# Kernel tuning notes

Measured on AMD Instinct MI355X. Metric: run time of the kernel, lower is better.

## Reference

```python
import jax, jax.numpy as jnp
import numpy as np

N_NODES = 100000
N_EDGES = 3200000
NEG_SLOPE = 0.01  # torch F.leaky_relu default


def _spmm(edge_src, edge_dst, edge_vals, x):
    # out[i] = sum_{e: dst[e]==i} vals[e] * x[src[e]]  ==  A @ x for COO A
    msgs = edge_vals[:, None] * x[edge_src]  # [E, D]
    return jax.ops.segment_sum(msgs, edge_dst, num_segments=N_NODES)


def _gcn_layer(x, edge_src, edge_dst, edge_vals, W, b):
    h = x @ W                      # dense GEMM [N, out]
    h = _spmm(edge_src, edge_dst, edge_vals, h)  # sparse aggregation
    h = h + b
    return jax.nn.leaky_relu(h, NEG_SLOPE)  # dropout=0 -> no-op


def setup_inputs() -> dict:
    key = jax.random.key(0)
    ks = jax.random.split(key, 10)
    nfeat, hid, ncls = 512, 256, 40
    features = jax.random.normal(ks[0], (N_NODES, nfeat), dtype=jnp.float32)
    edge_src = jax.random.randint(ks[1], (N_EDGES,), 0, N_NODES, dtype=jnp.int32)
    edge_dst = jax.random.randint(ks[2], (N_EDGES,), 0, N_NODES, dtype=jnp.int32)
    edge_vals = jax.random.uniform(ks[3], (N_EDGES,), dtype=jnp.float32)
    # init like torch: uniform(-stdv, stdv), stdv = 1/sqrt(out_features)
    def uinit(k, shape, out):
        s = 1.0 / np.sqrt(out)
        return jax.random.uniform(k, shape, minval=-s, maxval=s, dtype=jnp.float32)
    return {
        "features": features,
        "edge_src": edge_src,
        "edge_dst": edge_dst,
        "edge_vals": edge_vals,
        "W1": uinit(ks[4], (nfeat, hid), hid),
        "b1": uinit(ks[5], (hid,), hid),
        "Wh": uinit(ks[6], (hid, hid), hid),
        "bh": uinit(ks[7], (hid,), hid),
        "W2": uinit(ks[8], (hid, ncls), ncls),
        "b2": uinit(ks[9], (ncls,), ncls),
    }


def reference(features, edge_src, edge_dst, edge_vals, W1, b1, Wh, bh, W2, b2):
    x = _gcn_layer(features, edge_src, edge_dst, edge_vals, W1, b1)
    x = _gcn_layer(x, edge_src, edge_dst, edge_vals, Wh, bh)
    # output layer also uses default use_activation=True in the source
    x = _gcn_layer(x, edge_src, edge_dst, edge_vals, W2, b2)
    return x  # [N_NODES, nclasses]
```

## Files before the change

### kernel.cpp

```cpp
#include <hip/hip_runtime.h>

#define NEG_SLOPE 0.01f

typedef __attribute__((ext_vector_type(8))) short bf16x8;
typedef __attribute__((ext_vector_type(4))) float f32x4;

static __device__ __forceinline__ unsigned short f2bf(float f) {
  unsigned int u = __float_as_uint(f);
  return (unsigned short)((u + 0x7fffu + ((u >> 16) & 1u)) >> 16);
}
static __device__ __forceinline__ float bf2f(unsigned short s) {
  return __uint_as_float(((unsigned int)s) << 16);
}
static __device__ __forceinline__ float leaky(float r) { return r > 0.f ? r : r * NEG_SLOPE; }


__global__ __launch_bounds__(256) void zero_int_kernel(int* __restrict__ p, int n) {
  int i = blockIdx.x * 256 + threadIdx.x;
  if (i < n) p[i] = 0;
}

__global__ __launch_bounds__(256) void hist_kernel(const int* __restrict__ dst, int* __restrict__ cnt, int E) {
  int i = blockIdx.x * 256 + threadIdx.x;
  if (i < E) atomicAdd(&cnt[dst[i]], 1);
}

__global__ __launch_bounds__(256) void scan1_kernel(const int* __restrict__ cnt, int* __restrict__ rp,
                                                    int* __restrict__ bsum, int n) {
  __shared__ int sh[256];
  int t = threadIdx.x;
  int base = blockIdx.x * 2048 + t * 8;
  int v[8];
  int tot = 0;
#pragma unroll
  for (int j = 0; j < 8; ++j) {
    int i = base + j;
    int c = (i < n) ? cnt[i] : 0;
    v[j] = tot;
    tot += c;
  }
  sh[t] = tot;
  __syncthreads();
  for (int off = 1; off < 256; off <<= 1) {
    int x = sh[t];
    int y = (t >= off) ? sh[t - off] : 0;
    __syncthreads();
    sh[t] = x + y;
    __syncthreads();
  }
  int pre = sh[t] - tot;
#pragma unroll
  for (int j = 0; j < 8; ++j) {
    int i = base + j;
    if (i < n) rp[i] = pre + v[j];
  }
  if (t == 255) bsum[blockIdx.x] = sh[255];
}

__global__ void scan2_kernel(int* __restrict__ bsum, int nb, int* __restrict__ rp, int n) {
  if (threadIdx.x == 0 && blockIdx.x == 0) {
    int run = 0;
    for (int i = 0; i < nb; ++i) {
      int t = bsum[i];
      bsum[i] = run;
      run += t;
    }
    rp[n] = run;
  }
}

__global__ __launch_bounds__(256) void scan3_kernel(int* __restrict__ rp, const int* __restrict__ bsum,
                                                    int* __restrict__ cursor, int n) {
  int i = blockIdx.x * 256 + threadIdx.x;
  if (i < n) {
    int v = rp[i] + bsum[i >> 11];
    rp[i] = v;
    cursor[i] = v;
  }
}

__global__ __launch_bounds__(256) void scatter_kernel(const int* __restrict__ src, const int* __restrict__ dst,
                                                      const float* __restrict__ vals, int* __restrict__ cursor,
                                                      int* __restrict__ csrc, float* __restrict__ cval, int E) {
  int i = blockIdx.x * 256 + threadIdx.x;
  if (i < E) {
    int d = dst[i];
    int pos = atomicAdd(&cursor[d], 1);
    csrc[pos] = src[i];
    cval[pos] = vals[i];
  }
}


__global__ __launch_bounds__(256) void cvt_w_kernel(const float* __restrict__ W, unsigned short* __restrict__ Wt,
                                                    int K, int Nreal, int Npad) {
  int i = blockIdx.x * 256 + threadIdx.x;
  if (i >= Npad * K) return;
  int n = i / K, k = i - n * K;
  float v = (n < Nreal) ? W[(size_t)k * Nreal + n] : 0.f;
  Wt[i] = f2bf(v);
}


__global__ __launch_bounds__(256) void gemm_mfma_kernel(const float* __restrict__ A, const unsigned short* __restrict__ Wt,
                                                        unsigned short* __restrict__ C, int M, int N, int K) {
  __shared__ __align__(16) short As[128 * 72];
  __shared__ __align__(16) short Bs[64 * 72];
  const int t = threadIdx.x;
  const int lane = t & 63;
  const int w = t >> 6;
  const int wr = w >> 1;
  const int wc = w & 1;
  const int row0 = blockIdx.x * 128;
  const int col0 = blockIdx.y * 64;
  const int l15 = lane & 15;
  const int l16 = lane >> 4;

  f32x4 acc[4][2];
#pragma unroll
  for (int m = 0; m < 4; ++m)
#pragma unroll
    for (int n = 0; n < 2; ++n) acc[m][n] = (f32x4){0.f, 0.f, 0.f, 0.f};

  for (int k0 = 0; k0 < K; k0 += 64) {
    __syncthreads();
#pragma unroll
    for (int it = 0; it < 8; ++it) {
      int idx = it * 256 + t;
      int row = idx >> 4;
      int c4 = idx & 15;
      int grow = row0 + row;
      float4 v = make_float4(0.f, 0.f, 0.f, 0.f);
      if (grow < M) v = *(const float4*)&A[(size_t)grow * K + k0 + c4 * 4];
      unsigned int lo = (unsigned int)f2bf(v.x) | ((unsigned int)f2bf(v.y) << 16);
      unsigned int hi = (unsigned int)f2bf(v.z) | ((unsigned int)f2bf(v.w) << 16);
      *(uint2*)&As[row * 72 + c4 * 4] = make_uint2(lo, hi);
    }
#pragma unroll
    for (int it = 0; it < 2; ++it) {
      int idx = it * 256 + t;
      int n = idx >> 3;
      int c8 = idx & 7;
      uint4 v = *(const uint4*)&Wt[(size_t)(col0 + n) * K + k0 + c8 * 8];
      *(uint4*)&Bs[n * 72 + c8 * 8] = v;
    }
    __syncthreads();
#pragma unroll
    for (int kk = 0; kk < 64; kk += 32) {
      bf16x8 a[4], b[2];
#pragma unroll
      for (int m = 0; m < 4; ++m)
        a[m] = *(const bf16x8*)&As[(wr * 64 + m * 16 + l15) * 72 + kk + l16 * 8];
#pragma unroll
      for (int n = 0; n < 2; ++n)
        b[n] = *(const bf16x8*)&Bs[(wc * 32 + n * 16 + l15) * 72 + kk + l16 * 8];
#pragma unroll
      for (int m = 0; m < 4; ++m)
#pragma unroll
        for (int n = 0; n < 2; ++n)
          acc[m][n] = __builtin_amdgcn_mfma_f32_16x16x32_bf16(a[m], b[n], acc[m][n], 0, 0, 0);
    }
  }
#pragma unroll
  for (int m = 0; m < 4; ++m) {
#pragma unroll
    for (int j = 0; j < 4; ++j) {
      int grow = row0 + wr * 64 + m * 16 + l16 * 4 + j;
      if (grow < M) {
#pragma unroll
        for (int n = 0; n < 2; ++n) {
          int gcol = col0 + wc * 32 + n * 16 + l15;
          C[(size_t)grow * N + gcol] = f2bf(acc[m][n][j]);
        }
      }
    }
  }
}


__global__ __launch_bounds__(256) void spmm_d256_kernel(const unsigned short* __restrict__ x, const int* __restrict__ rp,
                                                        const int* __restrict__ csrc, const float* __restrict__ cval,
                                                        const float* __restrict__ bias, float* __restrict__ out, int n) {
  int node = blockIdx.x * 4 + (threadIdx.x >> 6);
  int lane = threadIdx.x & 63;
  if (node >= n) return;
  int s = rp[node], e = rp[node + 1];
  float a0 = 0.f, a1 = 0.f, a2 = 0.f, a3 = 0.f;
  int p = s;
  for (; p + 8 <= e; p += 8) {
    int srcs[8];
    float vals[8];
    uint2 rv[8];
#pragma unroll
    for (int q = 0; q < 8; ++q) {
      srcs[q] = csrc[p + q];
      vals[q] = cval[p + q];
    }
#pragma unroll
    for (int q = 0; q < 8; ++q)
      rv[q] = *(const uint2*)((const char*)x + (size_t)srcs[q] * 512 + lane * 8);
#pragma unroll
    for (int q = 0; q < 8; ++q) {
      a0 = fmaf(vals[q], __uint_as_float(rv[q].x << 16), a0);
      a1 = fmaf(vals[q], __uint_as_float(rv[q].x & 0xffff0000u), a1);
      a2 = fmaf(vals[q], __uint_as_float(rv[q].y << 16), a2);
      a3 = fmaf(vals[q], __uint_as_float(rv[q].y & 0xffff0000u), a3);
    }
  }
  for (; p < e; ++p) {
    int s0 = csrc[p];
    float v0 = cval[p];
    uint2 r = *(const uint2*)((const char*)x + (size_t)s0 * 512 + lane * 8);
    a0 = fmaf(v0, __uint_as_float(r.x << 16), a0);
    a1 = fmaf(v0, __uint_as_float(r.x & 0xffff0000u), a1);
    a2 = fmaf(v0, __uint_as_float(r.y << 16), a2);
    a3 = fmaf(v0, __uint_as_float(r.y & 0xffff0000u), a3);
  }
  float4 b = *(const float4*)&bias[lane * 4];
  float4 o;
  o.x = leaky(a0 + b.x);
  o.y = leaky(a1 + b.y);
  o.z = leaky(a2 + b.z);
  o.w = leaky(a3 + b.w);
  *(float4*)&out[(size_t)node * 256 + lane * 4] = o;
}


__global__ __launch_bounds__(256) void spmm_small_kernel(const unsigned short* __restrict__ x, const int* __restrict__ rp,
                                                         const int* __restrict__ csrc, const float* __restrict__ cval,
                                                         const float* __restrict__ bias, float* __restrict__ out,
                                                         int n, int D, int ldx) {
  int node = blockIdx.x * 4 + (threadIdx.x >> 6);
  int lane = threadIdx.x & 63;
  if (node >= n) return;
  int l = lane < D ? lane : 0;
  int s = rp[node], e = rp[node + 1];
  float acc = 0.f;
  int p = s;
  for (; p + 4 <= e; p += 4) {
    int s0 = csrc[p], s1 = csrc[p + 1], s2 = csrc[p + 2], s3 = csrc[p + 3];
    float v0 = cval[p], v1 = cval[p + 1], v2 = cval[p + 2], v3 = cval[p + 3];
    acc = fmaf(v0, bf2f(x[(size_t)s0 * ldx + l]), acc);
    acc = fmaf(v1, bf2f(x[(size_t)s1 * ldx + l]), acc);
    acc = fmaf(v2, bf2f(x[(size_t)s2 * ldx + l]), acc);
    acc = fmaf(v3, bf2f(x[(size_t)s3 * ldx + l]), acc);
  }
  for (; p < e; ++p) acc = fmaf(cval[p], bf2f(x[(size_t)csrc[p] * ldx + l]), acc);
  if (lane < D) {
    out[(size_t)node * D + lane] = leaky(acc + bias[lane]);
  }
}


extern "C" void kernel_launch(void* const* d_in, const int* in_sizes, int n_in,
                              void* d_out, int out_size, void* d_ws, size_t ws_size,
                              hipStream_t stream) {
  const float* features = (const float*)d_in[0];
  const int* esrc = (const int*)d_in[1];
  const int* edst = (const int*)d_in[2];
  const float* evals = (const float*)d_in[3];
  const float* W1 = (const float*)d_in[4];
  const float* b1 = (const float*)d_in[5];
  const float* Wh = (const float*)d_in[6];
  const float* bh = (const float*)d_in[7];
  const float* W2 = (const float*)d_in[8];
  const float* b2 = (const float*)d_in[9];

  const int E = in_sizes[1];
  const int hid = in_sizes[5];
  const int ncls = in_sizes[9];
  const int nfeat = in_sizes[4] / hid;
  const int Nn = in_sizes[0] / nfeat;
  const int nclsPad = 64;

  char* ws = (char*)d_ws;
  size_t off = 0;
  auto alloc = [&](size_t bytes) {
    char* p = ws + off;
    off += (bytes + 255) & ~(size_t)255;
    return p;
  };
  unsigned short* hA = (unsigned short*)alloc((size_t)Nn * hid * 2);
  float* hB = (float*)alloc((size_t)Nn * hid * 4);
  unsigned short* g3 = (unsigned short*)alloc((size_t)Nn * nclsPad * 2);
  unsigned short* Wt1 = (unsigned short*)alloc((size_t)hid * nfeat * 2);
  unsigned short* Wt2 = (unsigned short*)alloc((size_t)hid * hid * 2);
  unsigned short* Wt3 = (unsigned short*)alloc((size_t)nclsPad * hid * 2);
  int* rp = (int*)alloc((size_t)(Nn + 1) * 4);
  int* cursor = (int*)alloc((size_t)Nn * 4);
  int nb = (Nn + 2047) / 2048;
  int* bsum = (int*)alloc((size_t)nb * 4);
  int* csrc = (int*)alloc((size_t)E * 4);
  float* cval = (float*)alloc((size_t)E * 4);
  (void)ws_size;

  dim3 blk(256);

  zero_int_kernel<<<(Nn + 255) / 256, blk, 0, stream>>>(cursor, Nn);
  hist_kernel<<<(E + 255) / 256, blk, 0, stream>>>(edst, cursor, E);
  scan1_kernel<<<nb, blk, 0, stream>>>(cursor, rp, bsum, Nn);
  scan2_kernel<<<1, 64, 0, stream>>>(bsum, nb, rp, Nn);
  scan3_kernel<<<(Nn + 255) / 256, blk, 0, stream>>>(rp, bsum, cursor, Nn);
  scatter_kernel<<<(E + 255) / 256, blk, 0, stream>>>(esrc, edst, evals, cursor, csrc, cval, E);

  cvt_w_kernel<<<(hid * nfeat + 255) / 256, blk, 0, stream>>>(W1, Wt1, nfeat, hid, hid);
  cvt_w_kernel<<<(hid * hid + 255) / 256, blk, 0, stream>>>(Wh, Wt2, hid, hid, hid);
  cvt_w_kernel<<<(nclsPad * hid + 255) / 256, blk, 0, stream>>>(W2, Wt3, hid, ncls, nclsPad);

  int gm = (Nn + 127) / 128;

  gemm_mfma_kernel<<<dim3(gm, hid / 64), blk, 0, stream>>>(features, Wt1, hA, Nn, hid, nfeat);
  spmm_d256_kernel<<<(Nn + 3) / 4, blk, 0, stream>>>(hA, rp, csrc, cval, b1, hB, Nn);

  gemm_mfma_kernel<<<dim3(gm, hid / 64), blk, 0, stream>>>(hB, Wt2, hA, Nn, hid, hid);
  spmm_d256_kernel<<<(Nn + 3) / 4, blk, 0, stream>>>(hA, rp, csrc, cval, bh, hB, Nn);

  gemm_mfma_kernel<<<dim3(gm, nclsPad / 64), blk, 0, stream>>>(hB, Wt3, g3, Nn, nclsPad, hid);
  spmm_small_kernel<<<(Nn + 3) / 4, blk, 0, stream>>>(g3, rp, csrc, cval, b2, (float*)d_out, Nn, ncls, nclsPad);
}
```

Measured before the change: 1.378 ms.

## Store hidden activations as bf16 and widen GEMM tile to full output width

The SpMM kernels now write their hidden-layer outputs as bf16 instead of fp32, so the next GEMM reads half the bytes and loads them into shared memory without conversion. The GEMM is templated so one block covers all output columns (256 wide with 8 waves, or 64 wide with 2 waves). Each A row tile is then read from global memory once rather than once per column block. This cuts the redundant re-reads of features and hidden activations, at the cost of more accumulator registers per wave, fewer blocks, and an extra bf16 rounding of intermediate activations.

```diff
diff --git a/kernel.cpp b/kernel.cpp
--- a/kernel.cpp
+++ b/kernel.cpp
@@ -102,62 +102,76 @@
 }
 
 
-__global__ __launch_bounds__(256) void gemm_mfma_kernel(const float* __restrict__ A, const unsigned short* __restrict__ Wt,
-                                                        unsigned short* __restrict__ C, int M, int N, int K) {
+template <int BN, int WN, bool A_F32>
+__global__ __launch_bounds__(128 * WN) void gemm_bf16_kernel(const void* __restrict__ Ap,
+                                                             const unsigned short* __restrict__ Wt,
+                                                             unsigned short* __restrict__ C, int M, int K) {
+  constexpr int THREADS = 128 * WN;
   __shared__ __align__(16) short As[128 * 72];
-  __shared__ __align__(16) short Bs[64 * 72];
+  __shared__ __align__(16) short Bs[BN * 72];
   const int t = threadIdx.x;
   const int lane = t & 63;
   const int w = t >> 6;
-  const int wr = w >> 1;
-  const int wc = w & 1;
+  const int wr = w / WN;
+  const int wc = w % WN;
   const int row0 = blockIdx.x * 128;
-  const int col0 = blockIdx.y * 64;
   const int l15 = lane & 15;
   const int l16 = lane >> 4;
 
-  f32x4 acc[4][2];
+  f32x4 acc[4][4];
 #pragma unroll
   for (int m = 0; m < 4; ++m)
 #pragma unroll
-    for (int n = 0; n < 2; ++n) acc[m][n] = (f32x4){0.f, 0.f, 0.f, 0.f};
+    for (int n = 0; n < 4; ++n) acc[m][n] = (f32x4){0.f, 0.f, 0.f, 0.f};
 
   for (int k0 = 0; k0 < K; k0 += 64) {
     __syncthreads();
-#pragma unroll
-    for (int it = 0; it < 8; ++it) {
-      int idx = it * 256 + t;
-      int row = idx >> 4;
-      int c4 = idx & 15;
-      int grow = row0 + row;
-      float4 v = make_float4(0.f, 0.f, 0.f, 0.f);
-      if (grow < M) v = *(const float4*)&A[(size_t)grow * K + k0 + c4 * 4];
-      unsigned int lo = (unsigned int)f2bf(v.x) | ((unsigned int)f2bf(v.y) << 16);
-      unsigned int hi = (unsigned int)f2bf(v.z) | ((unsigned int)f2bf(v.w) << 16);
-      *(uint2*)&As[row * 72 + c4 * 4] = make_uint2(lo, hi);
-    }
-#pragma unroll
-    for (int it = 0; it < 2; ++it) {
-      int idx = it * 256 + t;
-      int n = idx >> 3;
-      int c8 = idx & 7;
-      uint4 v = *(const uint4*)&Wt[(size_t)(col0 + n) * K + k0 + c8 * 8];
+    if constexpr (A_F32) {
+      const float* A = (const float*)Ap;
+#pragma unroll
+      for (int it = 0; it < 2048 / THREADS; ++it) {
+        int idx = it * THREADS + t;
+        int row = idx >> 4, c4 = idx & 15;
+        int grow = row0 + row;
+        float4 v = make_float4(0.f, 0.f, 0.f, 0.f);
+        if (grow < M) v = *(const float4*)&A[(size_t)grow * K + k0 + c4 * 4];
+        unsigned int lo = (unsigned int)f2bf(v.x) | ((unsigned int)f2bf(v.y) << 16);
+        unsigned int hi = (unsigned int)f2bf(v.z) | ((unsigned int)f2bf(v.w) << 16);
+        *(uint2*)&As[row * 72 + c4 * 4] = make_uint2(lo, hi);
+      }
+    } else {
+      const unsigned short* A = (const unsigned short*)Ap;
+#pragma unroll
+      for (int it = 0; it < 1024 / THREADS; ++it) {
+        int idx = it * THREADS + t;
+        int row = idx >> 3, c8 = idx & 7;
+        int grow = row0 + row;
+        uint4 v = make_uint4(0u, 0u, 0u, 0u);
+        if (grow < M) v = *(const uint4*)&A[(size_t)grow * K + c8 * 8 + k0];
+        *(uint4*)&As[row * 72 + c8 * 8] = v;
+      }
+    }
+#pragma unroll
+    for (int it = 0; it < BN * 8 / THREADS; ++it) {
+      int idx = it * THREADS + t;
+      int n = idx >> 3, c8 = idx & 7;
+      uint4 v = *(const uint4*)&Wt[(size_t)n * K + k0 + c8 * 8];
       *(uint4*)&Bs[n * 72 + c8 * 8] = v;
     }
     __syncthreads();
 #pragma unroll
     for (int kk = 0; kk < 64; kk += 32) {
-      bf16x8 a[4], b[2];
+      bf16x8 a[4], b[4];
 #pragma unroll
       for (int m = 0; m < 4; ++m)
         a[m] = *(const bf16x8*)&As[(wr * 64 + m * 16 + l15) * 72 + kk + l16 * 8];
 #pragma unroll
-      for (int n = 0; n < 2; ++n)
-        b[n] = *(const bf16x8*)&Bs[(wc * 32 + n * 16 + l15) * 72 + kk + l16 * 8];
+      for (int n = 0; n < 4; ++n)
+        b[n] = *(const bf16x8*)&Bs[(wc * 64 + n * 16 + l15) * 72 + kk + l16 * 8];
 #pragma unroll
       for (int m = 0; m < 4; ++m)
 #pragma unroll
-        for (int n = 0; n < 2; ++n)
+        for (int n = 0; n < 4; ++n)
           acc[m][n] = __builtin_amdgcn_mfma_f32_16x16x32_bf16(a[m], b[n], acc[m][n], 0, 0, 0);
     }
   }
@@ -168,9 +182,9 @@
       int grow = row0 + wr * 64 + m * 16 + l16 * 4 + j;
       if (grow < M) {
 #pragma unroll
-        for (int n = 0; n < 2; ++n) {
-          int gcol = col0 + wc * 32 + n * 16 + l15;
-          C[(size_t)grow * N + gcol] = f2bf(acc[m][n][j]);
+        for (int n = 0; n < 4; ++n) {
+          int gcol = wc * 64 + n * 16 + l15;
+          C[(size_t)grow * BN + gcol] = f2bf(acc[m][n][j]);
         }
       }
     }
@@ -180,7 +194,8 @@
 
 __global__ __launch_bounds__(256) void spmm_d256_kernel(const unsigned short* __restrict__ x, const int* __restrict__ rp,
                                                         const int* __restrict__ csrc, const float* __restrict__ cval,
-                                                        const float* __restrict__ bias, float* __restrict__ out, int n) {
+                                                        const float* __restrict__ bias, unsigned short* __restrict__ out,
+                                                        int n) {
   int node = blockIdx.x * 4 + (threadIdx.x >> 6);
   int lane = threadIdx.x & 63;
   if (node >= n) return;
@@ -217,12 +232,9 @@
     a3 = fmaf(v0, __uint_as_float(r.y & 0xffff0000u), a3);
   }
   float4 b = *(const float4*)&bias[lane * 4];
-  float4 o;
-  o.x = leaky(a0 + b.x);
-  o.y = leaky(a1 + b.y);
-  o.z = leaky(a2 + b.z);
-  o.w = leaky(a3 + b.w);
-  *(float4*)&out[(size_t)node * 256 + lane * 4] = o;
+  unsigned int o01 = (unsigned int)f2bf(leaky(a0 + b.x)) | ((unsigned int)f2bf(leaky(a1 + b.y)) << 16);
+  unsigned int o23 = (unsigned int)f2bf(leaky(a2 + b.z)) | ((unsigned int)f2bf(leaky(a3 + b.w)) << 16);
+  *(uint2*)&out[(size_t)node * 256 + lane * 4] = make_uint2(o01, o23);
 }
 
 
@@ -281,7 +293,7 @@
     return p;
   };
   unsigned short* hA = (unsigned short*)alloc((size_t)Nn * hid * 2);
-  float* hB = (float*)alloc((size_t)Nn * hid * 4);
+  unsigned short* hB = (unsigned short*)alloc((size_t)Nn * hid * 2);
   unsigned short* g3 = (unsigned short*)alloc((size_t)Nn * nclsPad * 2);
   unsigned short* Wt1 = (unsigned short*)alloc((size_t)hid * nfeat * 2);
   unsigned short* Wt2 = (unsigned short*)alloc((size_t)hid * hid * 2);
@@ -309,12 +321,12 @@
 
   int gm = (Nn + 127) / 128;
 
-  gemm_mfma_kernel<<<dim3(gm, hid / 64), blk, 0, stream>>>(features, Wt1, hA, Nn, hid, nfeat);
+  gemm_bf16_kernel<256, 4, true><<<dim3(gm, 1), dim3(512), 0, stream>>>(features, Wt1, hA, Nn, nfeat);
   spmm_d256_kernel<<<(Nn + 3) / 4, blk, 0, stream>>>(hA, rp, csrc, cval, b1, hB, Nn);
 
-  gemm_mfma_kernel<<<dim3(gm, hid / 64), blk, 0, stream>>>(hB, Wt2, hA, Nn, hid, hid);
+  gemm_bf16_kernel<256, 4, false><<<dim3(gm, 1), dim3(512), 0, stream>>>(hB, Wt2, hA, Nn, hid);
   spmm_d256_kernel<<<(Nn + 3) / 4, blk, 0, stream>>>(hA, rp, csrc, cval, bh, hB, Nn);
 
-  gemm_mfma_kernel<<<dim3(gm, nclsPad / 64), blk, 0, stream>>>(hB, Wt3, g3, Nn, nclsPad, hid);
+  gemm_bf16_kernel<64, 1, false><<<dim3(gm, 1), dim3(128), 0, stream>>>(hB, Wt3, g3, Nn, hid);
   spmm_small_kernel<<<(Nn + 3) / 4, blk, 0, stream>>>(g3, rp, csrc, cval, b2, (float*)d_out, Nn, ncls, nclsPad);
 }
```

New measurement: 1.261 ms. 1.09x faster.
